# Optimization experiments

Measured on AMD Instinct MI355X. Metric: run time of the kernel, lower is better.

## Reference

```python
import jax, jax.numpy as jnp
import numpy as np

N_NODES = 100000
N_EDGES = 1600000
IN_CH = 128
HID = 128
OUT_CH = 10


def setup_inputs() -> dict:
    key = jax.random.key(0)
    ks = jax.random.split(key, 14)
    s_in = 1.0 / np.sqrt(IN_CH)
    s_h = 1.0 / np.sqrt(HID)
    return {
        "x0": jax.random.normal(ks[0], (N_NODES, IN_CH), jnp.float32),
        "edge_index": jax.random.randint(ks[1], (2, N_EDGES), 0, N_NODES, jnp.int32),
        "edge_weight": jax.random.uniform(ks[2], (N_EDGES,), jnp.float32),
        # GraphConv layer 1 (in -> hid): lin_rel (weight+bias) applied to aggregated msgs, lin_root (no bias)
        "W1_rel": jax.random.uniform(ks[3], (IN_CH, HID), jnp.float32, -s_in, s_in),
        "b1": jax.random.uniform(ks[4], (HID,), jnp.float32, -s_in, s_in),
        "W1_root": jax.random.uniform(ks[5], (IN_CH, HID), jnp.float32, -s_in, s_in),
        # GraphConv layer 2 (hid -> hid)
        "W2_rel": jax.random.uniform(ks[6], (HID, HID), jnp.float32, -s_h, s_h),
        "b2": jax.random.uniform(ks[7], (HID,), jnp.float32, -s_h, s_h),
        "W2_root": jax.random.uniform(ks[8], (HID, HID), jnp.float32, -s_h, s_h),
        # GraphConv layer 3 (hid -> hid)
        "W3_rel": jax.random.uniform(ks[9], (HID, HID), jnp.float32, -s_h, s_h),
        "b3": jax.random.uniform(ks[10], (HID,), jnp.float32, -s_h, s_h),
        "W3_root": jax.random.uniform(ks[11], (HID, HID), jnp.float32, -s_h, s_h),
        # classification head
        "W_lin": jax.random.uniform(ks[12], (HID, OUT_CH), jnp.float32, -s_h, s_h),
        "b_lin": jax.random.uniform(ks[13], (OUT_CH,), jnp.float32, -s_h, s_h),
    }


def _graph_conv(x, src, dst, ew, W_rel, b_rel, W_root):
    # message: x_j * w_e ; aggregate: scatter-add onto dst ; update: lin_rel(agg) + lin_root(x)
    msg = x[src] * ew[:, None]                                   # [E, C]
    agg = jax.ops.segment_sum(msg, dst, num_segments=x.shape[0])  # [N, C]
    return agg @ W_rel + b_rel + x @ W_root                      # [N, C']


def reference(x0, edge_index, edge_weight,
              W1_rel, b1, W1_root,
              W2_rel, b2, W2_root,
              W3_rel, b3, W3_root,
              W_lin, b_lin):
    src, dst = edge_index[0], edge_index[1]
    # dropout p=0.2 is identity in eval mode
    x1 = jax.nn.relu(_graph_conv(x0, src, dst, edge_weight, W1_rel, b1, W1_root))
    x2 = jax.nn.relu(_graph_conv(x1, src, dst, edge_weight, W2_rel, b2, W2_root))
    x3 = jax.nn.relu(_graph_conv(x2, src, dst, edge_weight, W3_rel, b3, W3_root))
    logits = x3 @ W_lin + b_lin
    return jax.nn.log_softmax(logits, axis=-1)
```

## Files before the change

kernel.cpp:

```cpp
#include <hip/hip_runtime.h>
#include <hip/hip_bf16.h>
#include <math.h>

#define C128 128
#define OUT_CH 10

typedef __attribute__((ext_vector_type(8))) short short8;
typedef __attribute__((ext_vector_type(4))) float f32x4;
typedef __attribute__((ext_vector_type(2))) float f32x2;
typedef __attribute__((ext_vector_type(4))) int i32x4;

__device__ __forceinline__ unsigned short f2bf(float f) {
    unsigned b = __float_as_uint(f);
    unsigned r = (b + 0x7FFF + ((b >> 16) & 1)) >> 16;
    return (unsigned short)r;
}
__device__ __forceinline__ float bf2f(unsigned short u) {
    return __uint_as_float(((unsigned)u) << 16);
}


#define NBMAX 400
#define BCAP  4608
#define P1K   4096

__global__ __launch_bounds__(512) void bin_kernel(
    const int* __restrict__ ei, const float* __restrict__ ew,
    int* __restrict__ gcur, unsigned* __restrict__ bins_rec,
    unsigned char* __restrict__ bins_dst, int E, int nb)
{
    __shared__ int cnt[NBMAX];
    __shared__ int pos[NBMAX];
    __shared__ int gbase[NBMAX];
    __shared__ int s[512];
    __shared__ int totalSh;
    __shared__ uint2 buf[P1K];

    const int t = threadIdx.x;
    const int e0 = blockIdx.x * P1K;

    for (int b = t; b < nb; b += 512) { cnt[b] = 0; pos[b] = 0; }
    __syncthreads();

    unsigned rec[8];
    int dstv[8];
    const int e = e0 + t * 8;
    if (e + 8 <= E) {
        i32x4 d0 = __builtin_nontemporal_load((const i32x4*)(ei + E + e));
        i32x4 d1 = __builtin_nontemporal_load((const i32x4*)(ei + E + e + 4));
        i32x4 s0 = __builtin_nontemporal_load((const i32x4*)(ei + e));
        i32x4 s1 = __builtin_nontemporal_load((const i32x4*)(ei + e + 4));
        f32x4 w0 = __builtin_nontemporal_load((const f32x4*)(ew + e));
        f32x4 w1 = __builtin_nontemporal_load((const f32x4*)(ew + e + 4));
        int dd[8] = {d0.x, d0.y, d0.z, d0.w, d1.x, d1.y, d1.z, d1.w};
        int ss[8] = {s0.x, s0.y, s0.z, s0.w, s1.x, s1.y, s1.z, s1.w};
        float ww[8] = {w0.x, w0.y, w0.z, w0.w, w1.x, w1.y, w1.z, w1.w};
#pragma unroll
        for (int j = 0; j < 8; ++j) {
            unsigned wb = __float_as_uint(ww[j]);
            unsigned r  = ((wb + 0x7FFF + ((wb >> 16) & 1)) >> 16) & 0x7FFFu;
            rec[j]  = (unsigned)ss[j] | (r << 17);
            dstv[j] = dd[j];
            atomicAdd(&cnt[dd[j] >> 8], 1);
        }
    } else {
#pragma unroll
        for (int j = 0; j < 8; ++j) {
            int ee = e + j;
            if (ee < E) {
                int dst = ei[E + ee];
                unsigned wb = __float_as_uint(ew[ee]);
                unsigned r  = ((wb + 0x7FFF + ((wb >> 16) & 1)) >> 16) & 0x7FFFu;
                rec[j]  = (unsigned)ei[ee] | (r << 17);
                dstv[j] = dst;
                atomicAdd(&cnt[dst >> 8], 1);
            } else {
                dstv[j] = -1;
            }
        }
    }
    __syncthreads();

    int c = (t < nb) ? cnt[t] : 0;
    s[t] = c;
    __syncthreads();
    for (int o = 1; o < 512; o <<= 1) {
        int u = (t >= o) ? s[t - o] : 0;
        __syncthreads();
        s[t] += u;
        __syncthreads();
    }
    if (t == nb - 1) totalSh = s[t];
    __syncthreads();

#pragma unroll
    for (int j = 0; j < 8; ++j) {
        if (dstv[j] >= 0) {
            int b = dstv[j] >> 8;
            int r = atomicAdd(&pos[b], 1);
            buf[s[b] - cnt[b] + r] = make_uint2(rec[j], (unsigned)dstv[j]);
        }
    }
    __syncthreads();

    if (t < nb) {
        int b = t + (int)((blockIdx.x * 131u) % (unsigned)nb);
        if (b >= nb) b -= nb;
        int cb = cnt[b];
        if (cb > 0) gbase[b] = atomicAdd(&gcur[b], cb);
    }
    __syncthreads();

    const int total = totalSh;
    for (int i = t; i < total; i += 512) {
        uint2 v = buf[i];
        int b = (int)(v.y >> 8);
        int dest = gbase[b] + (i - (s[b] - cnt[b]));
        if (dest < BCAP) {
            bins_rec[(size_t)b * BCAP + dest] = v.x;
            bins_dst[(size_t)b * BCAP + dest] = (unsigned char)(v.y & 255u);
        }
    }
}

__global__ __launch_bounds__(512) void bucket_scan_kernel(
    const int* __restrict__ gcur, int* __restrict__ bbase,
    int* __restrict__ row_ptr, int nb, int N, int E)
{
    __shared__ int s[512];
    int t = threadIdx.x;
    int v = (t < nb) ? gcur[t] : 0;
    s[t] = v;
    __syncthreads();
    for (int o = 1; o < 512; o <<= 1) {
        int u = (t >= o) ? s[t - o] : 0;
        __syncthreads();
        s[t] += u;
        __syncthreads();
    }
    if (t < nb) bbase[t] = s[t] - v;
    if (t == 0) row_ptr[N] = E;
}

__global__ __launch_bounds__(256) void build_kernel(
    const unsigned* __restrict__ bins_rec, const unsigned char* __restrict__ bins_dst,
    const int* __restrict__ gcur, const int* __restrict__ bbase,
    int* __restrict__ row_ptr, unsigned* __restrict__ csr, int N)
{
    __shared__ int rowCnt[256];
    __shared__ int rowOff[256];
    __shared__ int sc[256];
    __shared__ unsigned out[BCAP];

    const int b = blockIdx.x, t = threadIdx.x;
    int cnt = gcur[b];
    if (cnt > BCAP) cnt = BCAP;
    const int base = bbase[b];
    const unsigned* mbr = bins_rec + (size_t)b * BCAP;
    const unsigned char* mbd = bins_dst + (size_t)b * BCAP;

    rowCnt[t] = 0;
    __syncthreads();
    for (int i = t; i < cnt; i += 256) atomicAdd(&rowCnt[(int)mbd[i]], 1);
    __syncthreads();

    int v = rowCnt[t];
    sc[t] = v;
    __syncthreads();
    for (int o = 1; o < 256; o <<= 1) {
        int u = (t >= o) ? sc[t - o] : 0;
        __syncthreads();
        sc[t] += u;
        __syncthreads();
    }
    rowOff[t] = sc[t] - v;
    int idx = b * 256 + t;
    if (idx <= N) row_ptr[idx] = base + sc[t] - v;
    rowCnt[t] = 0;
    __syncthreads();

    for (int i = t; i < cnt; i += 256) {
        int d = (int)mbd[i];
        int k = atomicAdd(&rowCnt[d], 1);
        out[rowOff[d] + k] = mbr[i];
    }
    __syncthreads();

    for (int i = t; i < cnt; i += 256) csr[base + i] = out[i];
}


__global__ __launch_bounds__(256) void cvt_both_kernel(const float4* __restrict__ x,
                                                       ushort4* __restrict__ xb,
                                                       unsigned* __restrict__ xf8, int n4) {
    int i = blockIdx.x * blockDim.x + threadIdx.x;
    if (i < n4) {
        float4 v = x[i];
        ushort4 o;
        o.x = f2bf(v.x); o.y = f2bf(v.y); o.z = f2bf(v.z); o.w = f2bf(v.w);
        xb[i] = o;
        unsigned p = __builtin_amdgcn_cvt_pk_fp8_f32(v.x, v.y, 0, false);
        p = __builtin_amdgcn_cvt_pk_fp8_f32(v.z, v.w, p, true);
        xf8[i] = p;
    }
}


__global__ __launch_bounds__(256) void pack_all_kernel(
    const float* __restrict__ W1r, const float* __restrict__ W1t,
    const float* __restrict__ W2r, const float* __restrict__ W2t,
    const float* __restrict__ W3r, const float* __restrict__ W3t,
    const float* __restrict__ Wl,
    unsigned short* __restrict__ Wp1, unsigned short* __restrict__ Wp2,
    unsigned short* __restrict__ Wp3, unsigned short* __restrict__ WlP)
{
    int b = blockIdx.x;
    if (b < 384) {
        int which = b >> 7;
        const float* Wr = (which == 0) ? W1r : (which == 1) ? W2r : W3r;
        const float* Wt = (which == 0) ? W1t : (which == 1) ? W2t : W3t;
        unsigned short* Wp = (which == 0) ? Wp1 : (which == 1) ? Wp2 : Wp3;
        int idx = (b & 127) * 256 + threadIdx.x;
        int j    = idx & 7;
        int n    = (idx >> 3) & 127;
        int quad = (idx >> 10) & 3;
        int ks   = idx >> 12;
        const float* W = (ks < 4) ? Wr : Wt;
        int k = (ks & 3) * 32 + quad * 8 + j;
        Wp[idx] = f2bf(W[(size_t)k * C128 + n]);
    } else {
        int idx = (b - 384) * 256 + threadIdx.x;
        int j    = idx & 7;
        int col  = (idx >> 3) & 15;
        int quad = (idx >> 7) & 3;
        int ks   = (idx >> 9) & 3;
        int half = idx >> 11;
        int k = ks * 32 + quad * 8 + j;
        float v = (col < OUT_CH) ? Wl[(size_t)k * OUT_CH + col] : 0.f;
        unsigned short hi = f2bf(v);
        unsigned short outv = hi;
        if (half) outv = f2bf(v - bf2f(hi));
        WlP[idx] = outv;
    }
}


#define AGS 136

__global__ __launch_bounds__(256) void fused_layer(
    const unsigned* __restrict__ xf8,
    const int* __restrict__ row_ptr,
    const unsigned* __restrict__ csr,
    const unsigned short* __restrict__ xb,
    const unsigned short* __restrict__ Wp,
    const float* __restrict__ bias,
    unsigned short* __restrict__ outb, unsigned char* __restrict__ outf8, int N)
{
    __shared__ unsigned short AG[16 * AGS];
    __shared__ unsigned short XR[16 * AGS];

    const int t = threadIdx.x;
    const int w    = t >> 6;
    const int lane = t & 63;
    const int l16  = lane & 15;
    const int g    = lane >> 4;
    const int tile0 = blockIdx.x * 16;

    {
        int rrow = tile0 + w * 4 + g;
        int srow = (rrow < N) ? rrow : 0;
        uint4 v = *(const uint4*)&xb[(size_t)srow * C128 + l16 * 8];
        *(uint4*)&XR[(w * 4 + g) * AGS + l16 * 8] = v;
    }

    for (int i = 0; i < 4; ++i) {
        int node = tile0 + w * 4 + i;
        int i0 = 0, deg = 0;
        if (node < N) { i0 = row_ptr[node]; deg = row_ptr[node + 1] - i0; }

        f32x2 acc2[4];
#pragma unroll
        for (int j = 0; j < 4; ++j) acc2[j] = (f32x2){0.f, 0.f};

        for (int base = 0; base < deg; base += 64) {
            int rem = deg - base; if (rem > 64) rem = 64;
            int rec = 0;
            if (base + lane < deg)
                rec = (int)__builtin_nontemporal_load(&csr[i0 + base + lane]);

            for (int c = 0; c < rem; c += 16) {
                int i0e = c + g, i1e = c + 4 + g, i2e = c + 8 + g, i3e = c + 12 + g;
                int s0 = __shfl(rec, i0e & 63, 64);
                int s1 = __shfl(rec, i1e & 63, 64);
                int s2 = __shfl(rec, i2e & 63, 64);
                int s3 = __shfl(rec, i3e & 63, 64);
                float w0 = (i0e < rem) ? __uint_as_float(((unsigned)s0 >> 17) << 16) : 0.f;
                float w1 = (i1e < rem) ? __uint_as_float(((unsigned)s1 >> 17) << 16) : 0.f;
                float w2 = (i2e < rem) ? __uint_as_float(((unsigned)s2 >> 17) << 16) : 0.f;
                float w3 = (i3e < rem) ? __uint_as_float(((unsigned)s3 >> 17) << 16) : 0.f;
                uint2 q0 = *(const uint2*)&xf8[(unsigned)(s0 & 0x1FFFF) * 32u + l16 * 2];
                uint2 q1 = *(const uint2*)&xf8[(unsigned)(s1 & 0x1FFFF) * 32u + l16 * 2];
                uint2 q2 = *(const uint2*)&xf8[(unsigned)(s2 & 0x1FFFF) * 32u + l16 * 2];
                uint2 q3 = *(const uint2*)&xf8[(unsigned)(s3 & 0x1FFFF) * 32u + l16 * 2];
#define ACCUM(q, wv)                                                         \
                {                                                            \
                    f32x2 w2v = {(wv), (wv)};                                \
                    acc2[0] += __builtin_amdgcn_cvt_pk_f32_fp8((q).x, false) * w2v; \
                    acc2[1] += __builtin_amdgcn_cvt_pk_f32_fp8((q).x, true)  * w2v; \
                    acc2[2] += __builtin_amdgcn_cvt_pk_f32_fp8((q).y, false) * w2v; \
                    acc2[3] += __builtin_amdgcn_cvt_pk_f32_fp8((q).y, true)  * w2v; \
                }
                ACCUM(q0, w0) ACCUM(q1, w1) ACCUM(q2, w2) ACCUM(q3, w3)
#undef ACCUM
            }
        }

#pragma unroll
        for (int j = 0; j < 4; ++j) {
            acc2[j].x += __shfl_xor(acc2[j].x, 16, 64);
            acc2[j].y += __shfl_xor(acc2[j].y, 16, 64);
            acc2[j].x += __shfl_xor(acc2[j].x, 32, 64);
            acc2[j].y += __shfl_xor(acc2[j].y, 32, 64);
        }
        if (g == 0) {
            uint4 o;
            o.x = (unsigned)f2bf(acc2[0].x) | ((unsigned)f2bf(acc2[0].y) << 16);
            o.y = (unsigned)f2bf(acc2[1].x) | ((unsigned)f2bf(acc2[1].y) << 16);
            o.z = (unsigned)f2bf(acc2[2].x) | ((unsigned)f2bf(acc2[2].y) << 16);
            o.w = (unsigned)f2bf(acc2[3].x) | ((unsigned)f2bf(acc2[3].y) << 16);
            *(uint4*)&AG[(w * 4 + i) * AGS + l16 * 8] = o;
        }
    }
    __syncthreads();

    const int l15 = l16, quad = g;
    const int nt0 = 2 * w, nt1 = 2 * w + 1;
    float bv0 = bias[nt0 * 16 + l15];
    float bv1 = bias[nt1 * 16 + l15];
    f32x4 acc0 = (f32x4){0.f, 0.f, 0.f, 0.f};
    f32x4 acc1 = (f32x4){0.f, 0.f, 0.f, 0.f};

#pragma unroll
    for (int ks = 0; ks < 8; ++ks) {
        short8 a;
        if (ks < 4) a = *(const short8*)&AG[l15 * AGS + ks * 32 + quad * 8];
        else        a = *(const short8*)&XR[l15 * AGS + (ks - 4) * 32 + quad * 8];
        short8 b0 = *(const short8*)&Wp[(((ks * 4 + quad) * 128) + nt0 * 16 + l15) * 8];
        short8 b1 = *(const short8*)&Wp[(((ks * 4 + quad) * 128) + nt1 * 16 + l15) * 8];
        acc0 = __builtin_amdgcn_mfma_f32_16x16x32_bf16(a, b0, acc0, 0, 0, 0);
        acc1 = __builtin_amdgcn_mfma_f32_16x16x32_bf16(a, b1, acc1, 0, 0, 0);
    }

#pragma unroll
    for (int r = 0; r < 4; ++r) {
        int row = tile0 + quad * 4 + r;
        if (row < N) {
            float v0 = fmaxf(acc0[r] + bv0, 0.f);
            float v1 = fmaxf(acc1[r] + bv1, 0.f);
            outb[(size_t)row * C128 + nt0 * 16 + l15] = f2bf(v0);
            outb[(size_t)row * C128 + nt1 * 16 + l15] = f2bf(v1);
            unsigned p0 = __builtin_amdgcn_cvt_pk_fp8_f32(v0, 0.f, 0, false);
            unsigned p1 = __builtin_amdgcn_cvt_pk_fp8_f32(v1, 0.f, 0, false);
            outf8[(size_t)row * C128 + nt0 * 16 + l15] = (unsigned char)(p0 & 0xff);
            outf8[(size_t)row * C128 + nt1 * 16 + l15] = (unsigned char)(p1 & 0xff);
        }
    }
}


__global__ __launch_bounds__(256) void fused_layer_head(
    const unsigned* __restrict__ xf8,
    const int* __restrict__ row_ptr,
    const unsigned* __restrict__ csr,
    const unsigned short* __restrict__ xb,
    const unsigned short* __restrict__ Wp,
    const float* __restrict__ bias,
    const unsigned short* __restrict__ WlP, const float* __restrict__ bl,
    float* __restrict__ out, int N)
{
    __shared__ unsigned short AG[16 * AGS];
    __shared__ unsigned short XR[16 * AGS];

    const int t = threadIdx.x;
    const int w    = t >> 6;
    const int lane = t & 63;
    const int l16  = lane & 15;
    const int g    = lane >> 4;
    const int tile0 = blockIdx.x * 16;

    {
        int rrow = tile0 + w * 4 + g;
        int srow = (rrow < N) ? rrow : 0;
        uint4 v = *(const uint4*)&xb[(size_t)srow * C128 + l16 * 8];
        *(uint4*)&XR[(w * 4 + g) * AGS + l16 * 8] = v;
    }

    for (int i = 0; i < 4; ++i) {
        int node = tile0 + w * 4 + i;
        int i0 = 0, deg = 0;
        if (node < N) { i0 = row_ptr[node]; deg = row_ptr[node + 1] - i0; }

        f32x2 acc2[4];
#pragma unroll
        for (int j = 0; j < 4; ++j) acc2[j] = (f32x2){0.f, 0.f};

        for (int base = 0; base < deg; base += 64) {
            int rem = deg - base; if (rem > 64) rem = 64;
            int rec = 0;
            if (base + lane < deg)
                rec = (int)__builtin_nontemporal_load(&csr[i0 + base + lane]);

            for (int c = 0; c < rem; c += 16) {
                int i0e = c + g, i1e = c + 4 + g, i2e = c + 8 + g, i3e = c + 12 + g;
                int s0 = __shfl(rec, i0e & 63, 64);
                int s1 = __shfl(rec, i1e & 63, 64);
                int s2 = __shfl(rec, i2e & 63, 64);
                int s3 = __shfl(rec, i3e & 63, 64);
                float w0 = (i0e < rem) ? __uint_as_float(((unsigned)s0 >> 17) << 16) : 0.f;
                float w1 = (i1e < rem) ? __uint_as_float(((unsigned)s1 >> 17) << 16) : 0.f;
                float w2 = (i2e < rem) ? __uint_as_float(((unsigned)s2 >> 17) << 16) : 0.f;
                float w3 = (i3e < rem) ? __uint_as_float(((unsigned)s3 >> 17) << 16) : 0.f;
                uint2 q0 = *(const uint2*)&xf8[(unsigned)(s0 & 0x1FFFF) * 32u + l16 * 2];
                uint2 q1 = *(const uint2*)&xf8[(unsigned)(s1 & 0x1FFFF) * 32u + l16 * 2];
                uint2 q2 = *(const uint2*)&xf8[(unsigned)(s2 & 0x1FFFF) * 32u + l16 * 2];
                uint2 q3 = *(const uint2*)&xf8[(unsigned)(s3 & 0x1FFFF) * 32u + l16 * 2];
#define ACCUM(q, wv)                                                         \
                {                                                            \
                    f32x2 w2v = {(wv), (wv)};                                \
                    acc2[0] += __builtin_amdgcn_cvt_pk_f32_fp8((q).x, false) * w2v; \
                    acc2[1] += __builtin_amdgcn_cvt_pk_f32_fp8((q).x, true)  * w2v; \
                    acc2[2] += __builtin_amdgcn_cvt_pk_f32_fp8((q).y, false) * w2v; \
                    acc2[3] += __builtin_amdgcn_cvt_pk_f32_fp8((q).y, true)  * w2v; \
                }
                ACCUM(q0, w0) ACCUM(q1, w1) ACCUM(q2, w2) ACCUM(q3, w3)
#undef ACCUM
            }
        }

#pragma unroll
        for (int j = 0; j < 4; ++j) {
            acc2[j].x += __shfl_xor(acc2[j].x, 16, 64);
            acc2[j].y += __shfl_xor(acc2[j].y, 16, 64);
            acc2[j].x += __shfl_xor(acc2[j].x, 32, 64);
            acc2[j].y += __shfl_xor(acc2[j].y, 32, 64);
        }
        if (g == 0) {
            uint4 o;
            o.x = (unsigned)f2bf(acc2[0].x) | ((unsigned)f2bf(acc2[0].y) << 16);
            o.y = (unsigned)f2bf(acc2[1].x) | ((unsigned)f2bf(acc2[1].y) << 16);
            o.z = (unsigned)f2bf(acc2[2].x) | ((unsigned)f2bf(acc2[2].y) << 16);
            o.w = (unsigned)f2bf(acc2[3].x) | ((unsigned)f2bf(acc2[3].y) << 16);
            *(uint4*)&AG[(w * 4 + i) * AGS + l16 * 8] = o;
        }
    }
    __syncthreads();

    const int l15 = l16, quad = g;
    const int nt0 = 2 * w, nt1 = 2 * w + 1;
    float bv0 = bias[nt0 * 16 + l15];
    float bv1 = bias[nt1 * 16 + l15];
    f32x4 acc0 = (f32x4){0.f, 0.f, 0.f, 0.f};
    f32x4 acc1 = (f32x4){0.f, 0.f, 0.f, 0.f};

#pragma unroll
    for (int ks = 0; ks < 8; ++ks) {
        short8 a;
        if (ks < 4) a = *(const short8*)&AG[l15 * AGS + ks * 32 + quad * 8];
        else        a = *(const short8*)&XR[l15 * AGS + (ks - 4) * 32 + quad * 8];
        short8 b0 = *(const short8*)&Wp[(((ks * 4 + quad) * 128) + nt0 * 16 + l15) * 8];
        short8 b1 = *(const short8*)&Wp[(((ks * 4 + quad) * 128) + nt1 * 16 + l15) * 8];
        acc0 = __builtin_amdgcn_mfma_f32_16x16x32_bf16(a, b0, acc0, 0, 0, 0);
        acc1 = __builtin_amdgcn_mfma_f32_16x16x32_bf16(a, b1, acc1, 0, 0, 0);
    }

    __syncthreads();
#pragma unroll
    for (int r = 0; r < 4; ++r) {
        int lrow = quad * 4 + r;
        float v0 = fmaxf(acc0[r] + bv0, 0.f);
        float v1 = fmaxf(acc1[r] + bv1, 0.f);
        AG[lrow * AGS + nt0 * 16 + l15] = f2bf(v0);
        AG[lrow * AGS + nt1 * 16 + l15] = f2bf(v1);
    }
    __syncthreads();

    if (w == 0) {
        f32x4 hacc = (f32x4){0.f, 0.f, 0.f, 0.f};
#pragma unroll
        for (int ks = 0; ks < 4; ++ks) {
            short8 a2  = *(const short8*)&AG[l15 * AGS + ks * 32 + quad * 8];
            short8 bh  = *(const short8*)&WlP[(((ks * 4 + quad) * 16) + l15) * 8];
            short8 bl2 = *(const short8*)&WlP[2048 + (((ks * 4 + quad) * 16) + l15) * 8];
            hacc = __builtin_amdgcn_mfma_f32_16x16x32_bf16(a2, bh, hacc, 0, 0, 0);
            hacc = __builtin_amdgcn_mfma_f32_16x16x32_bf16(a2, bl2, hacc, 0, 0, 0);
        }
        float blv = (l15 < OUT_CH) ? bl[l15] : 0.f;
#pragma unroll
        for (int r = 0; r < 4; ++r) {
            int row = tile0 + quad * 4 + r;
            float lg = (l15 < OUT_CH) ? (hacc[r] + blv) : -1e30f;
            float m = lg;
            m = fmaxf(m, __shfl_xor(m, 1, 64));
            m = fmaxf(m, __shfl_xor(m, 2, 64));
            m = fmaxf(m, __shfl_xor(m, 4, 64));
            m = fmaxf(m, __shfl_xor(m, 8, 64));
            float s = __expf(lg - m);
            s += __shfl_xor(s, 1, 64);
            s += __shfl_xor(s, 2, 64);
            s += __shfl_xor(s, 4, 64);
            s += __shfl_xor(s, 8, 64);
            float lse = m + __logf(s);
            if (l15 < OUT_CH && row < N)
                out[(size_t)row * OUT_CH + l15] = lg - lse;
        }
    }
}


extern "C" void kernel_launch(void* const* d_in, const int* in_sizes, int n_in,
                              void* d_out, int out_size, void* d_ws, size_t ws_size,
                              hipStream_t stream) {
    const float* x0   = (const float*)d_in[0];
    const int*   ei   = (const int*)  d_in[1];
    const float* ew   = (const float*)d_in[2];
    const float* W1r  = (const float*)d_in[3];
    const float* b1   = (const float*)d_in[4];
    const float* W1t  = (const float*)d_in[5];
    const float* W2r  = (const float*)d_in[6];
    const float* b2   = (const float*)d_in[7];
    const float* W2t  = (const float*)d_in[8];
    const float* W3r  = (const float*)d_in[9];
    const float* b3   = (const float*)d_in[10];
    const float* W3t  = (const float*)d_in[11];
    const float* Wlin = (const float*)d_in[12];
    const float* blin = (const float*)d_in[13];

    const int N = in_sizes[0] / C128;
    const int E = in_sizes[1] / 2;
    const int nb = (N + 255) >> 8;

    char* ws = (char*)d_ws;
    size_t off = 0;
    auto alloc = [&](size_t bytes) {
        void* p = ws + off;
        off = (off + bytes + 255) & ~(size_t)255;
        return p;
    };
    size_t bb = (size_t)N * C128 * sizeof(unsigned short);
    size_t fb = (size_t)N * C128;
    unsigned short* xb0  = (unsigned short*)alloc(bb);
    unsigned short* xb1  = (unsigned short*)alloc(bb);
    unsigned char*  xf8a = (unsigned char*)alloc(fb);
    unsigned char*  xf8b = (unsigned char*)alloc(fb);
    unsigned short* Wp1  = (unsigned short*)alloc(32768 * 2);
    unsigned short* Wp2  = (unsigned short*)alloc(32768 * 2);
    unsigned short* Wp3  = (unsigned short*)alloc(32768 * 2);
    unsigned short* WlP  = (unsigned short*)alloc(4096 * 2);
    unsigned* csr  = (unsigned*)alloc((size_t)E * 4);
    int* row_ptr   = (int*)alloc((size_t)(N + 2) * 4);
    unsigned* bins_rec  = (unsigned*)alloc((size_t)nb * BCAP * 4);
    unsigned char* bins_dst = (unsigned char*)alloc((size_t)nb * BCAP);
    int* gcur      = (int*)alloc((size_t)nb * 4);
    int* bbase     = (int*)alloc((size_t)nb * 4);

    hipMemsetAsync(gcur, 0, (size_t)nb * sizeof(int), stream);
    bin_kernel<<<(E + P1K - 1) / P1K, 512, 0, stream>>>(ei, ew, gcur, bins_rec, bins_dst, E, nb);
    bucket_scan_kernel<<<1, 512, 0, stream>>>(gcur, bbase, row_ptr, nb, N, E);
    build_kernel<<<nb, 256, 0, stream>>>(bins_rec, bins_dst, gcur, bbase, row_ptr, csr, N);

    cvt_both_kernel<<<(N * C128 / 4 + 255) / 256, 256, 0, stream>>>(
        (const float4*)x0, (ushort4*)xb0, (unsigned*)xf8a, N * C128 / 4);
    pack_all_kernel<<<400, 256, 0, stream>>>(W1r, W1t, W2r, W2t, W3r, W3t, Wlin,
                                             Wp1, Wp2, Wp3, WlP);

    const int fusedGrid = (N + 15) / 16;

    fused_layer<<<fusedGrid, 256, 0, stream>>>(
        (const unsigned*)xf8a, row_ptr, csr, xb0, Wp1, b1, xb1, xf8b, N);
    fused_layer<<<fusedGrid, 256, 0, stream>>>(
        (const unsigned*)xf8b, row_ptr, csr, xb1, Wp2, b2, xb0, xf8a, N);
    fused_layer_head<<<fusedGrid, 256, 0, stream>>>(
        (const unsigned*)xf8a, row_ptr, csr, xb0, Wp3, b3, WlP, blin,
        (float*)d_out, N);
}
```

Before: 366.3 us.

## Use 8 waves per tile with 2 nodes each and prefetch CSR chunks

Fused layer kernels now launch 512 threads per block, so each of 8 waves gathers 2 nodes instead of 4 waves handling 4 nodes each. The row pointers and first 64 CSR records for both nodes are loaded up front, before any accumulation, so more gather loads are in flight. Each wave now computes one 16-column MFMA output tile instead of two. This is meant to raise memory-level parallelism in the latency-bound gather, at the cost of higher register pressure under the 512-thread launch bound and less work per wave in the GEMM step.

```diff
diff --git a/kernel.cpp b/kernel.cpp
--- a/kernel.cpp
+++ b/kernel.cpp
@@ -247,7 +247,98 @@
 
 #define AGS 136
 
-__global__ __launch_bounds__(256) void fused_layer(
+#define GATHER_BODY(rec_, rem_, acc2_)                                          \
+    for (int c = 0; c < (rem_); c += 16) {                                      \
+        int i0e = c + g, i1e = c + 4 + g, i2e = c + 8 + g, i3e = c + 12 + g;    \
+        int s0 = __shfl((rec_), i0e & 63, 64);                                  \
+        int s1 = __shfl((rec_), i1e & 63, 64);                                  \
+        int s2 = __shfl((rec_), i2e & 63, 64);                                  \
+        int s3 = __shfl((rec_), i3e & 63, 64);                                  \
+        float w0 = (i0e < (rem_)) ? __uint_as_float(((unsigned)s0 >> 17) << 16) : 0.f; \
+        float w1 = (i1e < (rem_)) ? __uint_as_float(((unsigned)s1 >> 17) << 16) : 0.f; \
+        float w2 = (i2e < (rem_)) ? __uint_as_float(((unsigned)s2 >> 17) << 16) : 0.f; \
+        float w3 = (i3e < (rem_)) ? __uint_as_float(((unsigned)s3 >> 17) << 16) : 0.f; \
+        uint2 q0 = *(const uint2*)&xf8[(unsigned)(s0 & 0x1FFFF) * 32u + l16 * 2]; \
+        uint2 q1 = *(const uint2*)&xf8[(unsigned)(s1 & 0x1FFFF) * 32u + l16 * 2]; \
+        uint2 q2 = *(const uint2*)&xf8[(unsigned)(s2 & 0x1FFFF) * 32u + l16 * 2]; \
+        uint2 q3 = *(const uint2*)&xf8[(unsigned)(s3 & 0x1FFFF) * 32u + l16 * 2]; \
+        { f32x2 w2v = {w0, w0};                                                 \
+          (acc2_)[0] += __builtin_amdgcn_cvt_pk_f32_fp8(q0.x, false) * w2v;     \
+          (acc2_)[1] += __builtin_amdgcn_cvt_pk_f32_fp8(q0.x, true)  * w2v;     \
+          (acc2_)[2] += __builtin_amdgcn_cvt_pk_f32_fp8(q0.y, false) * w2v;     \
+          (acc2_)[3] += __builtin_amdgcn_cvt_pk_f32_fp8(q0.y, true)  * w2v; }   \
+        { f32x2 w2v = {w1, w1};                                                 \
+          (acc2_)[0] += __builtin_amdgcn_cvt_pk_f32_fp8(q1.x, false) * w2v;     \
+          (acc2_)[1] += __builtin_amdgcn_cvt_pk_f32_fp8(q1.x, true)  * w2v;     \
+          (acc2_)[2] += __builtin_amdgcn_cvt_pk_f32_fp8(q1.y, false) * w2v;     \
+          (acc2_)[3] += __builtin_amdgcn_cvt_pk_f32_fp8(q1.y, true)  * w2v; }   \
+        { f32x2 w2v = {w2, w2};                                                 \
+          (acc2_)[0] += __builtin_amdgcn_cvt_pk_f32_fp8(q2.x, false) * w2v;     \
+          (acc2_)[1] += __builtin_amdgcn_cvt_pk_f32_fp8(q2.x, true)  * w2v;     \
+          (acc2_)[2] += __builtin_amdgcn_cvt_pk_f32_fp8(q2.y, false) * w2v;     \
+          (acc2_)[3] += __builtin_amdgcn_cvt_pk_f32_fp8(q2.y, true)  * w2v; }   \
+        { f32x2 w2v = {w3, w3};                                                 \
+          (acc2_)[0] += __builtin_amdgcn_cvt_pk_f32_fp8(q3.x, false) * w2v;     \
+          (acc2_)[1] += __builtin_amdgcn_cvt_pk_f32_fp8(q3.x, true)  * w2v;     \
+          (acc2_)[2] += __builtin_amdgcn_cvt_pk_f32_fp8(q3.y, false) * w2v;     \
+          (acc2_)[3] += __builtin_amdgcn_cvt_pk_f32_fp8(q3.y, true)  * w2v; }   \
+    }
+
+#define GATHER_PHASE                                                            \
+                                     \
+    if (w < 4) {                                                                \
+        int rrow = tile0 + w * 4 + g;                                           \
+        int srow = (rrow < N) ? rrow : 0;                                       \
+        uint4 v = *(const uint4*)&xb[(size_t)srow * C128 + l16 * 8];            \
+        *(uint4*)&XR[(w * 4 + g) * AGS + l16 * 8] = v;                          \
+    }                                                                           \
+                    \
+    int pi0[2], pdeg[2], prec[2];                                               \
+    _Pragma("unroll")                                                           \
+    for (int i = 0; i < 2; ++i) {                                               \
+        int node = tile0 + w * 2 + i;                                           \
+        int a = 0, d = 0;                                                       \
+        if (node < N) { a = row_ptr[node]; d = row_ptr[node + 1] - a; }         \
+        pi0[i] = a; pdeg[i] = d;                                                \
+    }                                                                           \
+    _Pragma("unroll")                                                           \
+    for (int i = 0; i < 2; ++i) {                                               \
+        prec[i] = 0;                                                            \
+        if (lane < pdeg[i])                                                     \
+            prec[i] = (int)__builtin_nontemporal_load(&csr[pi0[i] + lane]);     \
+    }                                                                           \
+    _Pragma("unroll")                                                           \
+    for (int i = 0; i < 2; ++i) {                                               \
+        int deg = pdeg[i];                                                      \
+        f32x2 acc2[4];                                                          \
+        acc2[0] = acc2[1] = acc2[2] = acc2[3] = (f32x2){0.f, 0.f};              \
+        int rem0 = (deg < 64) ? deg : 64;                                       \
+        GATHER_BODY(prec[i], rem0, acc2)                                        \
+        for (int base = 64; base < deg; base += 64) {                           \
+            int rem = deg - base; if (rem > 64) rem = 64;                       \
+            int rec = 0;                                                        \
+            if (base + lane < deg)                                              \
+                rec = (int)__builtin_nontemporal_load(&csr[pi0[i] + base + lane]); \
+            GATHER_BODY(rec, rem, acc2)                                         \
+        }                                                                       \
+        _Pragma("unroll")                                                       \
+        for (int j = 0; j < 4; ++j) {                                           \
+            acc2[j].x += __shfl_xor(acc2[j].x, 16, 64);                         \
+            acc2[j].y += __shfl_xor(acc2[j].y, 16, 64);                         \
+            acc2[j].x += __shfl_xor(acc2[j].x, 32, 64);                         \
+            acc2[j].y += __shfl_xor(acc2[j].y, 32, 64);                         \
+        }                                                                       \
+        if (g == 0) {                                                           \
+            uint4 o;                                                            \
+            o.x = (unsigned)f2bf(acc2[0].x) | ((unsigned)f2bf(acc2[0].y) << 16); \
+            o.y = (unsigned)f2bf(acc2[1].x) | ((unsigned)f2bf(acc2[1].y) << 16); \
+            o.z = (unsigned)f2bf(acc2[2].x) | ((unsigned)f2bf(acc2[2].y) << 16); \
+            o.w = (unsigned)f2bf(acc2[3].x) | ((unsigned)f2bf(acc2[3].y) << 16); \
+            *(uint4*)&AG[(w * 2 + i) * AGS + l16 * 8] = o;                      \
+        }                                                                       \
+    }
+
+__global__ __launch_bounds__(512) void fused_layer(
     const unsigned* __restrict__ xf8,
     const int* __restrict__ row_ptr,
     const unsigned* __restrict__ csr,
@@ -266,109 +357,36 @@
     const int g    = lane >> 4;
     const int tile0 = blockIdx.x * 16;
 
-    {
-        int rrow = tile0 + w * 4 + g;
-        int srow = (rrow < N) ? rrow : 0;
-        uint4 v = *(const uint4*)&xb[(size_t)srow * C128 + l16 * 8];
-        *(uint4*)&XR[(w * 4 + g) * AGS + l16 * 8] = v;
-    }
-
-    for (int i = 0; i < 4; ++i) {
-        int node = tile0 + w * 4 + i;
-        int i0 = 0, deg = 0;
-        if (node < N) { i0 = row_ptr[node]; deg = row_ptr[node + 1] - i0; }
-
-        f32x2 acc2[4];
-#pragma unroll
-        for (int j = 0; j < 4; ++j) acc2[j] = (f32x2){0.f, 0.f};
-
-        for (int base = 0; base < deg; base += 64) {
-            int rem = deg - base; if (rem > 64) rem = 64;
-            int rec = 0;
-            if (base + lane < deg)
-                rec = (int)__builtin_nontemporal_load(&csr[i0 + base + lane]);
-
-            for (int c = 0; c < rem; c += 16) {
-                int i0e = c + g, i1e = c + 4 + g, i2e = c + 8 + g, i3e = c + 12 + g;
-                int s0 = __shfl(rec, i0e & 63, 64);
-                int s1 = __shfl(rec, i1e & 63, 64);
-                int s2 = __shfl(rec, i2e & 63, 64);
-                int s3 = __shfl(rec, i3e & 63, 64);
-                float w0 = (i0e < rem) ? __uint_as_float(((unsigned)s0 >> 17) << 16) : 0.f;
-                float w1 = (i1e < rem) ? __uint_as_float(((unsigned)s1 >> 17) << 16) : 0.f;
-                float w2 = (i2e < rem) ? __uint_as_float(((unsigned)s2 >> 17) << 16) : 0.f;
-                float w3 = (i3e < rem) ? __uint_as_float(((unsigned)s3 >> 17) << 16) : 0.f;
-                uint2 q0 = *(const uint2*)&xf8[(unsigned)(s0 & 0x1FFFF) * 32u + l16 * 2];
-                uint2 q1 = *(const uint2*)&xf8[(unsigned)(s1 & 0x1FFFF) * 32u + l16 * 2];
-                uint2 q2 = *(const uint2*)&xf8[(unsigned)(s2 & 0x1FFFF) * 32u + l16 * 2];
-                uint2 q3 = *(const uint2*)&xf8[(unsigned)(s3 & 0x1FFFF) * 32u + l16 * 2];
-#define ACCUM(q, wv)                                                         \
-                {                                                            \
-                    f32x2 w2v = {(wv), (wv)};                                \
-                    acc2[0] += __builtin_amdgcn_cvt_pk_f32_fp8((q).x, false) * w2v; \
-                    acc2[1] += __builtin_amdgcn_cvt_pk_f32_fp8((q).x, true)  * w2v; \
-                    acc2[2] += __builtin_amdgcn_cvt_pk_f32_fp8((q).y, false) * w2v; \
-                    acc2[3] += __builtin_amdgcn_cvt_pk_f32_fp8((q).y, true)  * w2v; \
-                }
-                ACCUM(q0, w0) ACCUM(q1, w1) ACCUM(q2, w2) ACCUM(q3, w3)
-#undef ACCUM
-            }
-        }
-
-#pragma unroll
-        for (int j = 0; j < 4; ++j) {
-            acc2[j].x += __shfl_xor(acc2[j].x, 16, 64);
-            acc2[j].y += __shfl_xor(acc2[j].y, 16, 64);
-            acc2[j].x += __shfl_xor(acc2[j].x, 32, 64);
-            acc2[j].y += __shfl_xor(acc2[j].y, 32, 64);
-        }
-        if (g == 0) {
-            uint4 o;
-            o.x = (unsigned)f2bf(acc2[0].x) | ((unsigned)f2bf(acc2[0].y) << 16);
-            o.y = (unsigned)f2bf(acc2[1].x) | ((unsigned)f2bf(acc2[1].y) << 16);
-            o.z = (unsigned)f2bf(acc2[2].x) | ((unsigned)f2bf(acc2[2].y) << 16);
-            o.w = (unsigned)f2bf(acc2[3].x) | ((unsigned)f2bf(acc2[3].y) << 16);
-            *(uint4*)&AG[(w * 4 + i) * AGS + l16 * 8] = o;
-        }
-    }
+    GATHER_PHASE
     __syncthreads();
 
     const int l15 = l16, quad = g;
-    const int nt0 = 2 * w, nt1 = 2 * w + 1;
-    float bv0 = bias[nt0 * 16 + l15];
-    float bv1 = bias[nt1 * 16 + l15];
-    f32x4 acc0 = (f32x4){0.f, 0.f, 0.f, 0.f};
-    f32x4 acc1 = (f32x4){0.f, 0.f, 0.f, 0.f};
+    const int nt = w;
+    float bv = bias[nt * 16 + l15];
+    f32x4 acc = (f32x4){0.f, 0.f, 0.f, 0.f};
 
 #pragma unroll
     for (int ks = 0; ks < 8; ++ks) {
         short8 a;
         if (ks < 4) a = *(const short8*)&AG[l15 * AGS + ks * 32 + quad * 8];
         else        a = *(const short8*)&XR[l15 * AGS + (ks - 4) * 32 + quad * 8];
-        short8 b0 = *(const short8*)&Wp[(((ks * 4 + quad) * 128) + nt0 * 16 + l15) * 8];
-        short8 b1 = *(const short8*)&Wp[(((ks * 4 + quad) * 128) + nt1 * 16 + l15) * 8];
-        acc0 = __builtin_amdgcn_mfma_f32_16x16x32_bf16(a, b0, acc0, 0, 0, 0);
-        acc1 = __builtin_amdgcn_mfma_f32_16x16x32_bf16(a, b1, acc1, 0, 0, 0);
+        short8 b = *(const short8*)&Wp[(((ks * 4 + quad) * 128) + nt * 16 + l15) * 8];
+        acc = __builtin_amdgcn_mfma_f32_16x16x32_bf16(a, b, acc, 0, 0, 0);
     }
 
 #pragma unroll
     for (int r = 0; r < 4; ++r) {
         int row = tile0 + quad * 4 + r;
         if (row < N) {
-            float v0 = fmaxf(acc0[r] + bv0, 0.f);
-            float v1 = fmaxf(acc1[r] + bv1, 0.f);
-            outb[(size_t)row * C128 + nt0 * 16 + l15] = f2bf(v0);
-            outb[(size_t)row * C128 + nt1 * 16 + l15] = f2bf(v1);
-            unsigned p0 = __builtin_amdgcn_cvt_pk_fp8_f32(v0, 0.f, 0, false);
-            unsigned p1 = __builtin_amdgcn_cvt_pk_fp8_f32(v1, 0.f, 0, false);
-            outf8[(size_t)row * C128 + nt0 * 16 + l15] = (unsigned char)(p0 & 0xff);
-            outf8[(size_t)row * C128 + nt1 * 16 + l15] = (unsigned char)(p1 & 0xff);
-        }
-    }
-}
-
-
-__global__ __launch_bounds__(256) void fused_layer_head(
+            float v = fmaxf(acc[r] + bv, 0.f);
+            outb[(size_t)row * C128 + nt * 16 + l15] = f2bf(v);
+            unsigned p8 = __builtin_amdgcn_cvt_pk_fp8_f32(v, 0.f, 0, false);
+            outf8[(size_t)row * C128 + nt * 16 + l15] = (unsigned char)(p8 & 0xff);
+        }
+    }
+}
+
+__global__ __launch_bounds__(512) void fused_layer_head(
     const unsigned* __restrict__ xf8,
     const int* __restrict__ row_ptr,
     const unsigned* __restrict__ csr,
@@ -388,99 +406,29 @@
     const int g    = lane >> 4;
     const int tile0 = blockIdx.x * 16;
 
-    {
-        int rrow = tile0 + w * 4 + g;
-        int srow = (rrow < N) ? rrow : 0;
-        uint4 v = *(const uint4*)&xb[(size_t)srow * C128 + l16 * 8];
-        *(uint4*)&XR[(w * 4 + g) * AGS + l16 * 8] = v;
-    }
-
-    for (int i = 0; i < 4; ++i) {
-        int node = tile0 + w * 4 + i;
-        int i0 = 0, deg = 0;
-        if (node < N) { i0 = row_ptr[node]; deg = row_ptr[node + 1] - i0; }
-
-        f32x2 acc2[4];
-#pragma unroll
-        for (int j = 0; j < 4; ++j) acc2[j] = (f32x2){0.f, 0.f};
-
-        for (int base = 0; base < deg; base += 64) {
-            int rem = deg - base; if (rem > 64) rem = 64;
-            int rec = 0;
-            if (base + lane < deg)
-                rec = (int)__builtin_nontemporal_load(&csr[i0 + base + lane]);
-
-            for (int c = 0; c < rem; c += 16) {
-                int i0e = c + g, i1e = c + 4 + g, i2e = c + 8 + g, i3e = c + 12 + g;
-                int s0 = __shfl(rec, i0e & 63, 64);
-                int s1 = __shfl(rec, i1e & 63, 64);
-                int s2 = __shfl(rec, i2e & 63, 64);
-                int s3 = __shfl(rec, i3e & 63, 64);
-                float w0 = (i0e < rem) ? __uint_as_float(((unsigned)s0 >> 17) << 16) : 0.f;
-                float w1 = (i1e < rem) ? __uint_as_float(((unsigned)s1 >> 17) << 16) : 0.f;
-                float w2 = (i2e < rem) ? __uint_as_float(((unsigned)s2 >> 17) << 16) : 0.f;
-                float w3 = (i3e < rem) ? __uint_as_float(((unsigned)s3 >> 17) << 16) : 0.f;
-                uint2 q0 = *(const uint2*)&xf8[(unsigned)(s0 & 0x1FFFF) * 32u + l16 * 2];
-                uint2 q1 = *(const uint2*)&xf8[(unsigned)(s1 & 0x1FFFF) * 32u + l16 * 2];
-                uint2 q2 = *(const uint2*)&xf8[(unsigned)(s2 & 0x1FFFF) * 32u + l16 * 2];
-                uint2 q3 = *(const uint2*)&xf8[(unsigned)(s3 & 0x1FFFF) * 32u + l16 * 2];
-#define ACCUM(q, wv)                                                         \
-                {                                                            \
-                    f32x2 w2v = {(wv), (wv)};                                \
-                    acc2[0] += __builtin_amdgcn_cvt_pk_f32_fp8((q).x, false) * w2v; \
-                    acc2[1] += __builtin_amdgcn_cvt_pk_f32_fp8((q).x, true)  * w2v; \
-                    acc2[2] += __builtin_amdgcn_cvt_pk_f32_fp8((q).y, false) * w2v; \
-                    acc2[3] += __builtin_amdgcn_cvt_pk_f32_fp8((q).y, true)  * w2v; \
-                }
-                ACCUM(q0, w0) ACCUM(q1, w1) ACCUM(q2, w2) ACCUM(q3, w3)
-#undef ACCUM
-            }
-        }
-
-#pragma unroll
-        for (int j = 0; j < 4; ++j) {
-            acc2[j].x += __shfl_xor(acc2[j].x, 16, 64);
-            acc2[j].y += __shfl_xor(acc2[j].y, 16, 64);
-            acc2[j].x += __shfl_xor(acc2[j].x, 32, 64);
-            acc2[j].y += __shfl_xor(acc2[j].y, 32, 64);
-        }
-        if (g == 0) {
-            uint4 o;
-            o.x = (unsigned)f2bf(acc2[0].x) | ((unsigned)f2bf(acc2[0].y) << 16);
-            o.y = (unsigned)f2bf(acc2[1].x) | ((unsigned)f2bf(acc2[1].y) << 16);
-            o.z = (unsigned)f2bf(acc2[2].x) | ((unsigned)f2bf(acc2[2].y) << 16);
-            o.w = (unsigned)f2bf(acc2[3].x) | ((unsigned)f2bf(acc2[3].y) << 16);
-            *(uint4*)&AG[(w * 4 + i) * AGS + l16 * 8] = o;
-        }
-    }
+    GATHER_PHASE
     __syncthreads();
 
     const int l15 = l16, quad = g;
-    const int nt0 = 2 * w, nt1 = 2 * w + 1;
-    float bv0 = bias[nt0 * 16 + l15];
-    float bv1 = bias[nt1 * 16 + l15];
-    f32x4 acc0 = (f32x4){0.f, 0.f, 0.f, 0.f};
-    f32x4 acc1 = (f32x4){0.f, 0.f, 0.f, 0.f};
+    const int nt = w;
+    float bv = bias[nt * 16 + l15];
+    f32x4 acc = (f32x4){0.f, 0.f, 0.f, 0.f};
 
 #pragma unroll
     for (int ks = 0; ks < 8; ++ks) {
         short8 a;
         if (ks < 4) a = *(const short8*)&AG[l15 * AGS + ks * 32 + quad * 8];
         else        a = *(const short8*)&XR[l15 * AGS + (ks - 4) * 32 + quad * 8];
-        short8 b0 = *(const short8*)&Wp[(((ks * 4 + quad) * 128) + nt0 * 16 + l15) * 8];
-        short8 b1 = *(const short8*)&Wp[(((ks * 4 + quad) * 128) + nt1 * 16 + l15) * 8];
-        acc0 = __builtin_amdgcn_mfma_f32_16x16x32_bf16(a, b0, acc0, 0, 0, 0);
-        acc1 = __builtin_amdgcn_mfma_f32_16x16x32_bf16(a, b1, acc1, 0, 0, 0);
+        short8 b = *(const short8*)&Wp[(((ks * 4 + quad) * 128) + nt * 16 + l15) * 8];
+        acc = __builtin_amdgcn_mfma_f32_16x16x32_bf16(a, b, acc, 0, 0, 0);
     }
 
     __syncthreads();
 #pragma unroll
     for (int r = 0; r < 4; ++r) {
         int lrow = quad * 4 + r;
-        float v0 = fmaxf(acc0[r] + bv0, 0.f);
-        float v1 = fmaxf(acc1[r] + bv1, 0.f);
-        AG[lrow * AGS + nt0 * 16 + l15] = f2bf(v0);
-        AG[lrow * AGS + nt1 * 16 + l15] = f2bf(v1);
+        float v = fmaxf(acc[r] + bv, 0.f);
+        AG[lrow * AGS + nt * 16 + l15] = f2bf(v);
     }
     __syncthreads();
 
@@ -575,11 +523,11 @@
 
     const int fusedGrid = (N + 15) / 16;
 
-    fused_layer<<<fusedGrid, 256, 0, stream>>>(
+    fused_layer<<<fusedGrid, 512, 0, stream>>>(
         (const unsigned*)xf8a, row_ptr, csr, xb0, Wp1, b1, xb1, xf8b, N);
-    fused_layer<<<fusedGrid, 256, 0, stream>>>(
+    fused_layer<<<fusedGrid, 512, 0, stream>>>(
         (const unsigned*)xf8b, row_ptr, csr, xb1, Wp2, b2, xb0, xf8a, N);
-    fused_layer_head<<<fusedGrid, 256, 0, stream>>>(
+    fused_layer_head<<<fusedGrid, 512, 0, stream>>>(
         (const unsigned*)xf8a, row_ptr, csr, xb0, Wp3, b3, WlP, blin,
         (float*)d_out, N);
 }
```

Result: no change. 364.4 us (-0.5%).
